# Optimization experiments

Hardware: AMD Instinct MI355X
Metric: run time of the kernel (lower is better)

The kernel has to match this reference:

```python
import jax, jax.numpy as jnp
import numpy as np

N_TASKS = 3
N_SHARED = 4
N_TASK = 2
INP = 1024
EXPERT_DIM = 512


def setup_inputs() -> dict:
    key = jax.random.key(0)
    ks = jax.random.split(key, 7)
    s = 0.02
    task_inputs = jax.random.normal(ks[0], (N_TASKS, 16384, INP), dtype=jnp.float32)
    shared_W = jax.random.normal(ks[1], (N_SHARED, INP, EXPERT_DIM), dtype=jnp.float32) * s
    shared_b = jnp.zeros((N_SHARED, EXPERT_DIM), dtype=jnp.float32)
    task_W = jax.random.normal(ks[2], (N_TASKS, N_TASK, INP, EXPERT_DIM), dtype=jnp.float32) * s
    task_b = jnp.zeros((N_TASKS, N_TASK, EXPERT_DIM), dtype=jnp.float32)
    gate_W = jax.random.normal(ks[3], (N_TASKS, INP, N_SHARED + N_TASK), dtype=jnp.float32) * s
    gate_b = jnp.zeros((N_TASKS, N_SHARED + N_TASK), dtype=jnp.float32)
    return {
        'task_inputs': task_inputs,
        'shared_W': shared_W, 'shared_b': shared_b,
        'task_W': task_W, 'task_b': task_b,
        'gate_W': gate_W, 'gate_b': gate_b,
    }


def reference(task_inputs, shared_W, shared_b, task_W, task_b, gate_W, gate_b):
    # task_inputs: [T, B, I]
    x0 = task_inputs[0]  # shared experts always see task 0's input
    # shared experts: [B, E_s, O]
    shared_outs = jax.nn.relu(jnp.einsum('bi,eio->beo', x0, shared_W) + shared_b)
    # per-task experts: [T, B, E_t, O]
    task_outs = jax.nn.relu(jnp.einsum('tbi,teio->tbeo', task_inputs, task_W) + task_b[:, None, :, :])
    # stack shared + task experts -> [T, B, E_s+E_t, O]
    T = task_inputs.shape[0]
    all_outs = jnp.concatenate([
        jnp.broadcast_to(shared_outs[None], (T,) + shared_outs.shape),
        task_outs,
    ], axis=2)
    # gates: softmax over experts, [T, B, E_s+E_t]
    g = jax.nn.softmax(jnp.einsum('tbi,tig->tbg', task_inputs, gate_W) + gate_b[:, None, :], axis=-1)
    # gated weighted sum over experts -> [T, B, O]
    return jnp.einsum('tbeo,tbe->tbo', all_outs, g)
```

## Files before the change

kernel.cpp:

```cpp
#include <hip/hip_runtime.h>
#include <hip/hip_bf16.h>
#include <stdint.h>


#define TTASKS 3
#define BROWS  16384
#define KDIM   1024
#define ODIM   512
#define NGATE  6

typedef __attribute__((ext_vector_type(8))) __bf16 bf16x8;
typedef __attribute__((ext_vector_type(4))) float  f32x4;

#define XB_OFF 0
#define WT_OFF 100663296UL
#define GT_OFF 111149056UL
#define SH_OFF 112328704UL

#define MFMA_(a, bb, c) __builtin_amdgcn_mfma_f32_16x16x32_bf16(a, bb, c, 0, 0, 0)

__global__ __launch_bounds__(256) void cvt_inputs(const float* __restrict__ x,
                                                  __bf16* __restrict__ xb) {
  size_t i = ((size_t)blockIdx.x * 256 + threadIdx.x) * 8;
  const float4* p = (const float4*)(x + i);
  float4 a = p[0], b = p[1];
  bf16x8 o = { (__bf16)a.x, (__bf16)a.y, (__bf16)a.z, (__bf16)a.w,
               (__bf16)b.x, (__bf16)b.y, (__bf16)b.z, (__bf16)b.w };
  *(bf16x8*)(xb + i) = o;
}

__global__ __launch_bounds__(256) void cvt_weights(const float* __restrict__ shW,
                                                   const float* __restrict__ tkW,
                                                   __bf16* __restrict__ wT) {
  int s = blockIdx.z;
  const float* src = (s < 4) ? (shW + (size_t)s * KDIM * ODIM)
                             : (tkW + (size_t)(s - 4) * KDIM * ODIM);
  int o   = blockIdx.x * 64 + (threadIdx.x & 63);
  int sub = threadIdx.x >> 6;
#pragma unroll
  for (int kk = 0; kk < 2; ++kk) {
    int k0 = blockIdx.y * 64 + (sub * 2 + kk) * 8;
    bf16x8 v;
#pragma unroll
    for (int i = 0; i < 8; ++i)
      v[i] = (__bf16)src[(size_t)(k0 + i) * ODIM + o];
    *(bf16x8*)(wT + ((size_t)s * ODIM + o) * KDIM + k0) = v;
  }
}

__global__ __launch_bounds__(256) void gates_kernel(const __bf16* __restrict__ xb,
                                                    const float* __restrict__ gW,
                                                    const float* __restrict__ gb,
                                                    float* __restrict__ gates) {
  int w = blockIdx.x * 4 + (threadIdx.x >> 6);
  int lane = threadIdx.x & 63;
  int t = w >> 14, b = w & (BROWS - 1);
  const __bf16* xr = xb + ((size_t)t * BROWS + b) * KDIM;
  const float* gw = gW + (size_t)t * KDIM * NGATE;
  float d[NGATE] = {0.f, 0.f, 0.f, 0.f, 0.f, 0.f};
#pragma unroll
  for (int i = 0; i < 2; ++i) {
    int k0 = (i * 64 + lane) * 8;
    bf16x8 xv = *(const bf16x8*)(xr + k0);
#pragma unroll
    for (int kk = 0; kk < 8; ++kk) {
      float xf = (float)xv[kk];
#pragma unroll
      for (int j = 0; j < NGATE; ++j) d[j] += xf * gw[(k0 + kk) * NGATE + j];
    }
  }
#pragma unroll
  for (int j = 0; j < NGATE; ++j) {
#pragma unroll
    for (int off = 32; off > 0; off >>= 1) d[j] += __shfl_xor(d[j], off, 64);
    d[j] += gb[t * NGATE + j];
  }
  float m = d[0];
#pragma unroll
  for (int j = 1; j < NGATE; ++j) m = fmaxf(m, d[j]);
  float s = 0.f;
#pragma unroll
  for (int j = 0; j < NGATE; ++j) { d[j] = expf(d[j] - m); s += d[j]; }
  float inv = 1.f / s;
  if (lane < NGATE) {
    float v = d[0];
#pragma unroll
    for (int j = 1; j < NGATE; ++j) v = (lane == j) ? d[j] : v;
    gates[(size_t)w * NGATE + lane] = v * inv;
  }
}

__device__ __forceinline__ void gemm_128(const __bf16* __restrict__ Ap,
                                         const __bf16* __restrict__ Bp,
                                         __bf16* As, __bf16* Bs,
                                         f32x4 acc[4][4]) {
  const int tid = threadIdx.x, lane = tid & 63, wv = tid >> 6;
  const int wm = wv >> 1, wn = wv & 1;
  const int lr = lane & 15, lg = lane >> 4, x7 = lr & 7;

  for (int kt = 0; kt < 16; ++kt) {
    const int k0 = kt * 64;
#pragma unroll
    for (int it = 0; it < 4; ++it) {
      const int idx = it * 256 + tid;
      const int r   = idx >> 3;
      const int cs  = (idx & 7) ^ (r & 7);
      __builtin_amdgcn_global_load_lds(
          (const __attribute__((address_space(1))) void*)(Ap + (size_t)r * KDIM + k0 + cs * 8),
          (__attribute__((address_space(3))) void*)(As + (it * 256 + wv * 64) * 8), 16, 0, 0);
      __builtin_amdgcn_global_load_lds(
          (const __attribute__((address_space(1))) void*)(Bp + (size_t)r * KDIM + k0 + cs * 8),
          (__attribute__((address_space(3))) void*)(Bs + (it * 256 + wv * 64) * 8), 16, 0, 0);
    }
    __syncthreads();

    const __bf16* aB = As + (wm * 64 + lr) * 64;
    const __bf16* bB = Bs + (wn * 64 + lr) * 64;
#pragma unroll
    for (int ks = 0; ks < 2; ++ks) {
      const int xo = ((ks * 4 + lg) ^ x7) * 8;
      bf16x8 af[4], bf[4];
#pragma unroll
      for (int mi = 0; mi < 4; ++mi) af[mi] = *(const bf16x8*)(aB + mi * 16 * 64 + xo);
#pragma unroll
      for (int ni = 0; ni < 4; ++ni) bf[ni] = *(const bf16x8*)(bB + ni * 16 * 64 + xo);
#pragma unroll
      for (int mi = 0; mi < 4; ++mi)
#pragma unroll
        for (int ni = 0; ni < 4; ++ni)
          acc[mi][ni] = MFMA_(af[mi], bf[ni], acc[mi][ni]);
    }
    __syncthreads();
  }
}

__global__ __launch_bounds__(256, 2) void shared_gemm(const __bf16* __restrict__ xb0,
                                                      const __bf16* __restrict__ wT,
                                                      const float* __restrict__ shb,
                                                      __bf16* __restrict__ shOut) {
  __shared__ __align__(16) __bf16 As[128 * 64], Bs[128 * 64];
  const int e = blockIdx.z;
  const int rowBase = blockIdx.x * 128, colBase = blockIdx.y * 128;
  const int tid = threadIdx.x, lane = tid & 63, wv = tid >> 6;
  const int wm = wv >> 1, wn = wv & 1, lr = lane & 15, lg = lane >> 4;

  f32x4 acc[4][4];
  f32x4 z = {0.f, 0.f, 0.f, 0.f};
#pragma unroll
  for (int mi = 0; mi < 4; ++mi)
#pragma unroll
    for (int ni = 0; ni < 4; ++ni) acc[mi][ni] = z;

  gemm_128(xb0 + (size_t)rowBase * KDIM,
           wT + ((size_t)e * ODIM + colBase) * KDIM, As, Bs, acc);

#pragma unroll
  for (int ni = 0; ni < 4; ++ni) {
    int col = colBase + wn * 64 + ni * 16 + lr;
    float bias = shb[e * ODIM + col];
#pragma unroll
    for (int mi = 0; mi < 4; ++mi)
#pragma unroll
      for (int r = 0; r < 4; ++r) {
        int row = rowBase + wm * 64 + mi * 16 + lg * 4 + r;
        float v = fmaxf(acc[mi][ni][r] + bias, 0.f);
        shOut[((size_t)e * BROWS + row) * ODIM + col] = (__bf16)v;
      }
  }
}

__global__ __launch_bounds__(256, 2) void taskA_gemm(const __bf16* __restrict__ xb,
                                                     const __bf16* __restrict__ wT,
                                                     const float* __restrict__ tkb,
                                                     const float* __restrict__ gates,
                                                     const __bf16* __restrict__ shOut,
                                                     float* __restrict__ out) {
  __shared__ __align__(16) __bf16 As[128 * 64], Bs[128 * 64];
  const int t = blockIdx.z;
  const int rowBase = blockIdx.x * 128, colBase = blockIdx.y * 128;
  const int tid = threadIdx.x, lane = tid & 63, wv = tid >> 6;
  const int wm = wv >> 1, wn = wv & 1, lr = lane & 15, lg = lane >> 4;
  const size_t NB = (size_t)BROWS * ODIM;

  f32x4 acc[4][4];
  f32x4 z = {0.f, 0.f, 0.f, 0.f};
#pragma unroll
  for (int mi = 0; mi < 4; ++mi)
#pragma unroll
    for (int ni = 0; ni < 4; ++ni) acc[mi][ni] = z;

  gemm_128(xb + ((size_t)t * BROWS + rowBase) * KDIM,
           wT + ((size_t)(4 + t * 2) * ODIM + colBase) * KDIM, As, Bs, acc);

#pragma unroll
  for (int mi = 0; mi < 4; ++mi)
#pragma unroll
    for (int r = 0; r < 4; ++r) {
      int row = rowBase + wm * 64 + mi * 16 + lg * 4 + r;
      const float* gp = gates + ((size_t)t * BROWS + row) * NGATE;
      float g0 = gp[0], g1 = gp[1], g2 = gp[2], g3 = gp[3], g4 = gp[4];
#pragma unroll
      for (int ni = 0; ni < 4; ++ni) {
        int col = colBase + wn * 64 + ni * 16 + lr;
        size_t rc = (size_t)row * ODIM + col;
        float s = g0 * (float)shOut[rc] + g1 * (float)shOut[NB + rc] +
                  g2 * (float)shOut[2 * NB + rc] + g3 * (float)shOut[3 * NB + rc];
        float bias = tkb[(t * 2) * ODIM + col];
        s += g4 * fmaxf(acc[mi][ni][r] + bias, 0.f);
        out[((size_t)t * BROWS + row) * ODIM + col] = s;
      }
    }
}

__global__ __launch_bounds__(256, 2) void taskB_gemm(const __bf16* __restrict__ xb,
                                                     const __bf16* __restrict__ wT,
                                                     const float* __restrict__ tkb,
                                                     const float* __restrict__ gates,
                                                     float* __restrict__ out) {
  __shared__ __align__(16) __bf16 As[128 * 64], Bs[128 * 64];
  const int t = blockIdx.z;
  const int rowBase = blockIdx.x * 128, colBase = blockIdx.y * 128;
  const int tid = threadIdx.x, lane = tid & 63, wv = tid >> 6;
  const int wm = wv >> 1, wn = wv & 1, lr = lane & 15, lg = lane >> 4;

  f32x4 acc[4][4];
  f32x4 z = {0.f, 0.f, 0.f, 0.f};
#pragma unroll
  for (int mi = 0; mi < 4; ++mi)
#pragma unroll
    for (int ni = 0; ni < 4; ++ni) acc[mi][ni] = z;

  gemm_128(xb + ((size_t)t * BROWS + rowBase) * KDIM,
           wT + ((size_t)(4 + t * 2 + 1) * ODIM + colBase) * KDIM, As, Bs, acc);

#pragma unroll
  for (int mi = 0; mi < 4; ++mi)
#pragma unroll
    for (int r = 0; r < 4; ++r) {
      int row = rowBase + wm * 64 + mi * 16 + lg * 4 + r;
      float g5 = gates[((size_t)t * BROWS + row) * NGATE + 5];
#pragma unroll
      for (int ni = 0; ni < 4; ++ni) {
        int col = colBase + wn * 64 + ni * 16 + lr;
        float bias = tkb[(t * 2 + 1) * ODIM + col];
        size_t oi = ((size_t)t * BROWS + row) * ODIM + col;
        out[oi] += g5 * fmaxf(acc[mi][ni][r] + bias, 0.f);
      }
    }
}

extern "C" void kernel_launch(void* const* d_in, const int* in_sizes, int n_in,
                              void* d_out, int out_size, void* d_ws, size_t ws_size,
                              hipStream_t stream) {
  const float* x   = (const float*)d_in[0];
  const float* shW = (const float*)d_in[1];
  const float* shb = (const float*)d_in[2];
  const float* tkW = (const float*)d_in[3];
  const float* tkb = (const float*)d_in[4];
  const float* gW  = (const float*)d_in[5];
  const float* gb  = (const float*)d_in[6];
  float* out = (float*)d_out;
  (void)in_sizes; (void)n_in; (void)out_size; (void)ws_size;

  char* ws = (char*)d_ws;
  __bf16* xb    = (__bf16*)(ws + XB_OFF);
  __bf16* wT    = (__bf16*)(ws + WT_OFF);
  float*  gates = (float*) (ws + GT_OFF);
  __bf16* shOut = (__bf16*)(ws + SH_OFF);

  cvt_inputs <<<dim3(24576), 256, 0, stream>>>(x, xb);
  cvt_weights<<<dim3(8, 16, 10), 256, 0, stream>>>(shW, tkW, wT);
  gates_kernel<<<dim3((TTASKS * BROWS) / 4), 256, 0, stream>>>(xb, gW, gb, gates);

  shared_gemm<<<dim3(BROWS / 128, ODIM / 128, 4), 256, 0, stream>>>(xb, wT, shb, shOut);
  taskA_gemm <<<dim3(BROWS / 128, ODIM / 128, TTASKS), 256, 0, stream>>>(xb, wT, tkb, gates,
                                                                         shOut, out);
  taskB_gemm <<<dim3(BROWS / 128, ODIM / 128, TTASKS), 256, 0, stream>>>(xb, wT, tkb, gates,
                                                                         out);
}
```

Measured before the change: 649.6 us.

## Fuse gate computation into input conversion and merge expert GEMM kernels

Input conversion and gate softmax now share one kernel, so the bf16 input is not re-read to compute gates. Task 0 computes all six experts (four shared plus its two) in one block, accumulating the gated output in registers while still writing the shared outputs. Tasks 1 and 2 now run both task experts in one kernel that reuses the staged A tile for two B tiles, which removes the read-modify-write of the output. The cost is more registers and LDS per block, and the task-0 kernel runs as a long serial grid with a single z-slice.

```diff
diff --git a/kernel.cpp b/kernel.cpp
--- a/kernel.cpp
+++ b/kernel.cpp
@@ -19,14 +19,59 @@
 
 #define MFMA_(a, bb, c) __builtin_amdgcn_mfma_f32_16x16x32_bf16(a, bb, c, 0, 0, 0)
 
-__global__ __launch_bounds__(256) void cvt_inputs(const float* __restrict__ x,
-                                                  __bf16* __restrict__ xb) {
-  size_t i = ((size_t)blockIdx.x * 256 + threadIdx.x) * 8;
-  const float4* p = (const float4*)(x + i);
-  float4 a = p[0], b = p[1];
-  bf16x8 o = { (__bf16)a.x, (__bf16)a.y, (__bf16)a.z, (__bf16)a.w,
-               (__bf16)b.x, (__bf16)b.y, (__bf16)b.z, (__bf16)b.w };
-  *(bf16x8*)(xb + i) = o;
+__global__ __launch_bounds__(256) void cvt_gates(const float* __restrict__ x,
+                                                 __bf16* __restrict__ xb,
+                                                 const float* __restrict__ gW,
+                                                 const float* __restrict__ gb,
+                                                 float* __restrict__ gates) {
+  const int w = blockIdx.x * 4 + (threadIdx.x >> 6);
+  const int lane = threadIdx.x & 63;
+  const int t = w >> 14;
+  const float* xr = x + (size_t)w * KDIM;
+  const float* gw = gW + (size_t)t * KDIM * NGATE;
+
+  const int k0 = lane * 16;
+  float4 f[4];
+#pragma unroll
+  for (int i = 0; i < 4; ++i) f[i] = *(const float4*)(xr + k0 + i * 4);
+  bf16x8 o0 = { (__bf16)f[0].x, (__bf16)f[0].y, (__bf16)f[0].z, (__bf16)f[0].w,
+                (__bf16)f[1].x, (__bf16)f[1].y, (__bf16)f[1].z, (__bf16)f[1].w };
+  bf16x8 o1 = { (__bf16)f[2].x, (__bf16)f[2].y, (__bf16)f[2].z, (__bf16)f[2].w,
+                (__bf16)f[3].x, (__bf16)f[3].y, (__bf16)f[3].z, (__bf16)f[3].w };
+  *(bf16x8*)(xb + (size_t)w * KDIM + k0)     = o0;
+  *(bf16x8*)(xb + (size_t)w * KDIM + k0 + 8) = o1;
+
+  float d[NGATE] = {0.f, 0.f, 0.f, 0.f, 0.f, 0.f};
+#pragma unroll
+  for (int kk = 0; kk < 16; ++kk) {
+    float xf = ((const float*)f)[kk];
+    const float* gr = gw + (size_t)(k0 + kk) * NGATE;
+    float2 ga = *(const float2*)(gr);
+    float2 gbv = *(const float2*)(gr + 2);
+    float2 gc = *(const float2*)(gr + 4);
+    d[0] += xf * ga.x;  d[1] += xf * ga.y;
+    d[2] += xf * gbv.x; d[3] += xf * gbv.y;
+    d[4] += xf * gc.x;  d[5] += xf * gc.y;
+  }
+#pragma unroll
+  for (int j = 0; j < NGATE; ++j) {
+#pragma unroll
+    for (int off = 32; off > 0; off >>= 1) d[j] += __shfl_xor(d[j], off, 64);
+    d[j] += gb[t * NGATE + j];
+  }
+  float m = d[0];
+#pragma unroll
+  for (int j = 1; j < NGATE; ++j) m = fmaxf(m, d[j]);
+  float s = 0.f;
+#pragma unroll
+  for (int j = 0; j < NGATE; ++j) { d[j] = expf(d[j] - m); s += d[j]; }
+  float inv = 1.f / s;
+  if (lane < NGATE) {
+    float v = d[0];
+#pragma unroll
+    for (int j = 1; j < NGATE; ++j) v = (lane == j) ? d[j] : v;
+    gates[(size_t)w * NGATE + lane] = v * inv;
+  }
 }
 
 __global__ __launch_bounds__(256) void cvt_weights(const float* __restrict__ shW,
@@ -48,45 +93,16 @@
   }
 }
 
-__global__ __launch_bounds__(256) void gates_kernel(const __bf16* __restrict__ xb,
-                                                    const float* __restrict__ gW,
-                                                    const float* __restrict__ gb,
-                                                    float* __restrict__ gates) {
-  int w = blockIdx.x * 4 + (threadIdx.x >> 6);
-  int lane = threadIdx.x & 63;
-  int t = w >> 14, b = w & (BROWS - 1);
-  const __bf16* xr = xb + ((size_t)t * BROWS + b) * KDIM;
-  const float* gw = gW + (size_t)t * KDIM * NGATE;
-  float d[NGATE] = {0.f, 0.f, 0.f, 0.f, 0.f, 0.f};
-#pragma unroll
-  for (int i = 0; i < 2; ++i) {
-    int k0 = (i * 64 + lane) * 8;
-    bf16x8 xv = *(const bf16x8*)(xr + k0);
-#pragma unroll
-    for (int kk = 0; kk < 8; ++kk) {
-      float xf = (float)xv[kk];
-#pragma unroll
-      for (int j = 0; j < NGATE; ++j) d[j] += xf * gw[(k0 + kk) * NGATE + j];
-    }
-  }
-#pragma unroll
-  for (int j = 0; j < NGATE; ++j) {
-#pragma unroll
-    for (int off = 32; off > 0; off >>= 1) d[j] += __shfl_xor(d[j], off, 64);
-    d[j] += gb[t * NGATE + j];
-  }
-  float m = d[0];
-#pragma unroll
-  for (int j = 1; j < NGATE; ++j) m = fmaxf(m, d[j]);
-  float s = 0.f;
-#pragma unroll
-  for (int j = 0; j < NGATE; ++j) { d[j] = expf(d[j] - m); s += d[j]; }
-  float inv = 1.f / s;
-  if (lane < NGATE) {
-    float v = d[0];
-#pragma unroll
-    for (int j = 1; j < NGATE; ++j) v = (lane == j) ? d[j] : v;
-    gates[(size_t)w * NGATE + lane] = v * inv;
+__device__ __forceinline__ void stage_tile(const __bf16* __restrict__ g,
+                                           __bf16* lds, int tid, int wv) {
+#pragma unroll
+  for (int it = 0; it < 4; ++it) {
+    const int idx = it * 256 + tid;
+    const int r   = idx >> 3;
+    const int cs  = (idx & 7) ^ (r & 7);
+    __builtin_amdgcn_global_load_lds(
+        (const __attribute__((address_space(1))) void*)(g + (size_t)r * KDIM + cs * 8),
+        (__attribute__((address_space(3))) void*)(lds + (it * 256 + wv * 64) * 8), 16, 0, 0);
   }
 }
 
@@ -99,21 +115,9 @@
   const int lr = lane & 15, lg = lane >> 4, x7 = lr & 7;
 
   for (int kt = 0; kt < 16; ++kt) {
-    const int k0 = kt * 64;
-#pragma unroll
-    for (int it = 0; it < 4; ++it) {
-      const int idx = it * 256 + tid;
-      const int r   = idx >> 3;
-      const int cs  = (idx & 7) ^ (r & 7);
-      __builtin_amdgcn_global_load_lds(
-          (const __attribute__((address_space(1))) void*)(Ap + (size_t)r * KDIM + k0 + cs * 8),
-          (__attribute__((address_space(3))) void*)(As + (it * 256 + wv * 64) * 8), 16, 0, 0);
-      __builtin_amdgcn_global_load_lds(
-          (const __attribute__((address_space(1))) void*)(Bp + (size_t)r * KDIM + k0 + cs * 8),
-          (__attribute__((address_space(3))) void*)(Bs + (it * 256 + wv * 64) * 8), 16, 0, 0);
-    }
+    stage_tile(Ap + kt * 64, As, tid, wv);
+    stage_tile(Bp + kt * 64, Bs, tid, wv);
     __syncthreads();
-
     const __bf16* aB = As + (wm * 64 + lr) * 64;
     const __bf16* bB = Bs + (wn * 64 + lr) * 64;
 #pragma unroll
@@ -134,63 +138,121 @@
   }
 }
 
-__global__ __launch_bounds__(256, 2) void shared_gemm(const __bf16* __restrict__ xb0,
-                                                      const __bf16* __restrict__ wT,
-                                                      const float* __restrict__ shb,
-                                                      __bf16* __restrict__ shOut) {
+__global__ __launch_bounds__(256, 2) void task0_shared(const __bf16* __restrict__ xb0,
+                                                       const __bf16* __restrict__ wT,
+                                                       const float* __restrict__ shb,
+                                                       const float* __restrict__ tkb,
+                                                       const float* __restrict__ gates,
+                                                       __bf16* __restrict__ shOut,
+                                                       float* __restrict__ out) {
   __shared__ __align__(16) __bf16 As[128 * 64], Bs[128 * 64];
-  const int e = blockIdx.z;
   const int rowBase = blockIdx.x * 128, colBase = blockIdx.y * 128;
   const int tid = threadIdx.x, lane = tid & 63, wv = tid >> 6;
   const int wm = wv >> 1, wn = wv & 1, lr = lane & 15, lg = lane >> 4;
-
-  f32x4 acc[4][4];
-  f32x4 z = {0.f, 0.f, 0.f, 0.f};
+  const __bf16* Ap = xb0 + (size_t)rowBase * KDIM;
+
+  float outv[4][4][4];
 #pragma unroll
   for (int mi = 0; mi < 4; ++mi)
 #pragma unroll
-    for (int ni = 0; ni < 4; ++ni) acc[mi][ni] = z;
-
-  gemm_128(xb0 + (size_t)rowBase * KDIM,
-           wT + ((size_t)e * ODIM + colBase) * KDIM, As, Bs, acc);
+    for (int ni = 0; ni < 4; ++ni)
+#pragma unroll
+      for (int r = 0; r < 4; ++r) outv[mi][ni][r] = 0.f;
+
+#pragma unroll 1
+  for (int e = 0; e < 6; ++e) {
+    f32x4 acc[4][4];
+    f32x4 z = {0.f, 0.f, 0.f, 0.f};
+#pragma unroll
+    for (int mi = 0; mi < 4; ++mi)
+#pragma unroll
+      for (int ni = 0; ni < 4; ++ni) acc[mi][ni] = z;
+
+    gemm_128(Ap, wT + ((size_t)e * ODIM + colBase) * KDIM, As, Bs, acc);
+
+    const float* bias_p = (e < 4) ? (shb + e * ODIM) : (tkb + (e - 4) * ODIM);
+#pragma unroll
+    for (int ni = 0; ni < 4; ++ni) {
+      int col = colBase + wn * 64 + ni * 16 + lr;
+      float bias = bias_p[col];
+#pragma unroll
+      for (int mi = 0; mi < 4; ++mi)
+#pragma unroll
+        for (int r = 0; r < 4; ++r) {
+          int row = rowBase + wm * 64 + mi * 16 + lg * 4 + r;
+          float v = fmaxf(acc[mi][ni][r] + bias, 0.f);
+          if (e < 4)
+            shOut[((size_t)e * BROWS + row) * ODIM + col] = (__bf16)v;
+          outv[mi][ni][r] += gates[(size_t)row * NGATE + e] * v;
+        }
+    }
+  }
 
 #pragma unroll
   for (int ni = 0; ni < 4; ++ni) {
     int col = colBase + wn * 64 + ni * 16 + lr;
-    float bias = shb[e * ODIM + col];
 #pragma unroll
     for (int mi = 0; mi < 4; ++mi)
 #pragma unroll
       for (int r = 0; r < 4; ++r) {
         int row = rowBase + wm * 64 + mi * 16 + lg * 4 + r;
-        float v = fmaxf(acc[mi][ni][r] + bias, 0.f);
-        shOut[((size_t)e * BROWS + row) * ODIM + col] = (__bf16)v;
+        out[(size_t)row * ODIM + col] = outv[mi][ni][r];
       }
   }
 }
 
-__global__ __launch_bounds__(256, 2) void taskA_gemm(const __bf16* __restrict__ xb,
-                                                     const __bf16* __restrict__ wT,
-                                                     const float* __restrict__ tkb,
-                                                     const float* __restrict__ gates,
-                                                     const __bf16* __restrict__ shOut,
-                                                     float* __restrict__ out) {
-  __shared__ __align__(16) __bf16 As[128 * 64], Bs[128 * 64];
-  const int t = blockIdx.z;
+__global__ __launch_bounds__(256, 2) void task12_pair(const __bf16* __restrict__ xb,
+                                                      const __bf16* __restrict__ wT,
+                                                      const float* __restrict__ tkb,
+                                                      const float* __restrict__ gates,
+                                                      const __bf16* __restrict__ shOut,
+                                                      float* __restrict__ out) {
+  __shared__ __align__(16) __bf16 As[128 * 64], Bs0[128 * 64], Bs1[128 * 64];
+  const int t = 1 + blockIdx.z;
   const int rowBase = blockIdx.x * 128, colBase = blockIdx.y * 128;
   const int tid = threadIdx.x, lane = tid & 63, wv = tid >> 6;
-  const int wm = wv >> 1, wn = wv & 1, lr = lane & 15, lg = lane >> 4;
+  const int wm = wv >> 1, wn = wv & 1, lr = lane & 15, lg = lane >> 4, x7 = lr & 7;
   const size_t NB = (size_t)BROWS * ODIM;
 
-  f32x4 acc[4][4];
+  const __bf16* Ap  = xb + ((size_t)t * BROWS + rowBase) * KDIM;
+  const __bf16* Bp0 = wT + ((size_t)(4 + t * 2) * ODIM + colBase) * KDIM;
+  const __bf16* Bp1 = wT + ((size_t)(4 + t * 2 + 1) * ODIM + colBase) * KDIM;
+
+  f32x4 acc0[4][4], acc1[4][4];
   f32x4 z = {0.f, 0.f, 0.f, 0.f};
 #pragma unroll
   for (int mi = 0; mi < 4; ++mi)
 #pragma unroll
-    for (int ni = 0; ni < 4; ++ni) acc[mi][ni] = z;
-
-  gemm_128(xb + ((size_t)t * BROWS + rowBase) * KDIM,
-           wT + ((size_t)(4 + t * 2) * ODIM + colBase) * KDIM, As, Bs, acc);
+    for (int ni = 0; ni < 4; ++ni) { acc0[mi][ni] = z; acc1[mi][ni] = z; }
+
+  for (int kt = 0; kt < 16; ++kt) {
+    stage_tile(Ap  + kt * 64, As,  tid, wv);
+    stage_tile(Bp0 + kt * 64, Bs0, tid, wv);
+    stage_tile(Bp1 + kt * 64, Bs1, tid, wv);
+    __syncthreads();
+    const __bf16* aB  = As  + (wm * 64 + lr) * 64;
+    const __bf16* bB0 = Bs0 + (wn * 64 + lr) * 64;
+    const __bf16* bB1 = Bs1 + (wn * 64 + lr) * 64;
+#pragma unroll
+    for (int ks = 0; ks < 2; ++ks) {
+      const int xo = ((ks * 4 + lg) ^ x7) * 8;
+      bf16x8 af[4], bf0[4], bf1[4];
+#pragma unroll
+      for (int mi = 0; mi < 4; ++mi) af[mi]  = *(const bf16x8*)(aB  + mi * 16 * 64 + xo);
+#pragma unroll
+      for (int ni = 0; ni < 4; ++ni) bf0[ni] = *(const bf16x8*)(bB0 + ni * 16 * 64 + xo);
+#pragma unroll
+      for (int ni = 0; ni < 4; ++ni) bf1[ni] = *(const bf16x8*)(bB1 + ni * 16 * 64 + xo);
+#pragma unroll
+      for (int mi = 0; mi < 4; ++mi)
+#pragma unroll
+        for (int ni = 0; ni < 4; ++ni) {
+          acc0[mi][ni] = MFMA_(af[mi], bf0[ni], acc0[mi][ni]);
+          acc1[mi][ni] = MFMA_(af[mi], bf1[ni], acc1[mi][ni]);
+        }
+    }
+    __syncthreads();
+  }
 
 #pragma unroll
   for (int mi = 0; mi < 4; ++mi)
@@ -198,53 +260,16 @@
     for (int r = 0; r < 4; ++r) {
       int row = rowBase + wm * 64 + mi * 16 + lg * 4 + r;
       const float* gp = gates + ((size_t)t * BROWS + row) * NGATE;
-      float g0 = gp[0], g1 = gp[1], g2 = gp[2], g3 = gp[3], g4 = gp[4];
+      float g0 = gp[0], g1 = gp[1], g2 = gp[2], g3 = gp[3], g4 = gp[4], g5 = gp[5];
 #pragma unroll
       for (int ni = 0; ni < 4; ++ni) {
         int col = colBase + wn * 64 + ni * 16 + lr;
         size_t rc = (size_t)row * ODIM + col;
         float s = g0 * (float)shOut[rc] + g1 * (float)shOut[NB + rc] +
                   g2 * (float)shOut[2 * NB + rc] + g3 * (float)shOut[3 * NB + rc];
-        float bias = tkb[(t * 2) * ODIM + col];
-        s += g4 * fmaxf(acc[mi][ni][r] + bias, 0.f);
+        s += g4 * fmaxf(acc0[mi][ni][r] + tkb[(t * 2) * ODIM + col], 0.f);
+        s += g5 * fmaxf(acc1[mi][ni][r] + tkb[(t * 2 + 1) * ODIM + col], 0.f);
         out[((size_t)t * BROWS + row) * ODIM + col] = s;
-      }
-    }
-}
-
-__global__ __launch_bounds__(256, 2) void taskB_gemm(const __bf16* __restrict__ xb,
-                                                     const __bf16* __restrict__ wT,
-                                                     const float* __restrict__ tkb,
-                                                     const float* __restrict__ gates,
-                                                     float* __restrict__ out) {
-  __shared__ __align__(16) __bf16 As[128 * 64], Bs[128 * 64];
-  const int t = blockIdx.z;
-  const int rowBase = blockIdx.x * 128, colBase = blockIdx.y * 128;
-  const int tid = threadIdx.x, lane = tid & 63, wv = tid >> 6;
-  const int wm = wv >> 1, wn = wv & 1, lr = lane & 15, lg = lane >> 4;
-
-  f32x4 acc[4][4];
-  f32x4 z = {0.f, 0.f, 0.f, 0.f};
-#pragma unroll
-  for (int mi = 0; mi < 4; ++mi)
-#pragma unroll
-    for (int ni = 0; ni < 4; ++ni) acc[mi][ni] = z;
-
-  gemm_128(xb + ((size_t)t * BROWS + rowBase) * KDIM,
-           wT + ((size_t)(4 + t * 2 + 1) * ODIM + colBase) * KDIM, As, Bs, acc);
-
-#pragma unroll
-  for (int mi = 0; mi < 4; ++mi)
-#pragma unroll
-    for (int r = 0; r < 4; ++r) {
-      int row = rowBase + wm * 64 + mi * 16 + lg * 4 + r;
-      float g5 = gates[((size_t)t * BROWS + row) * NGATE + 5];
-#pragma unroll
-      for (int ni = 0; ni < 4; ++ni) {
-        int col = colBase + wn * 64 + ni * 16 + lr;
-        float bias = tkb[(t * 2 + 1) * ODIM + col];
-        size_t oi = ((size_t)t * BROWS + row) * ODIM + col;
-        out[oi] += g5 * fmaxf(acc[mi][ni][r] + bias, 0.f);
       }
     }
 }
@@ -268,13 +293,11 @@
   float*  gates = (float*) (ws + GT_OFF);
   __bf16* shOut = (__bf16*)(ws + SH_OFF);
 
-  cvt_inputs <<<dim3(24576), 256, 0, stream>>>(x, xb);
+  cvt_gates  <<<dim3((TTASKS * BROWS) / 4), 256, 0, stream>>>(x, xb, gW, gb, gates);
   cvt_weights<<<dim3(8, 16, 10), 256, 0, stream>>>(shW, tkW, wT);
-  gates_kernel<<<dim3((TTASKS * BROWS) / 4), 256, 0, stream>>>(xb, gW, gb, gates);
-
-  shared_gemm<<<dim3(BROWS / 128, ODIM / 128, 4), 256, 0, stream>>>(xb, wT, shb, shOut);
-  taskA_gemm <<<dim3(BROWS / 128, ODIM / 128, TTASKS), 256, 0, stream>>>(xb, wT, tkb, gates,
-                                                                         shOut, out);
-  taskB_gemm <<<dim3(BROWS / 128, ODIM / 128, TTASKS), 256, 0, stream>>>(xb, wT, tkb, gates,
-                                                                         out);
-}
+
+  task0_shared<<<dim3(BROWS / 128, ODIM / 128), 256, 0, stream>>>(xb, wT, shb, tkb,
+                                                                  gates, shOut, out);
+  task12_pair <<<dim3(BROWS / 128, ODIM / 128, 2), 256, 0, stream>>>(xb, wT, tkb, gates,
+                                                                     shOut, out);
+}
```

Measured after the change: 653.7 us. Within noise of the previous version (+0.6%).
